# Performance work log

Measured on AMD Instinct MI355X. Metric: run time of the kernel, lower is better.

The kernel has to match this reference:

```python
import jax, jax.numpy as jnp
import numpy as np

EPS = 1e-12          # sinkhorn_knopp epsilon
LOW, HIGH = 0.02, 0.98  # SquashedSigmoid bounds
N_ITERS = 10         # num_iterations
BATCH = 2097152


def setup_inputs() -> dict:
    key = jax.random.key(0)
    ks = jax.random.split(key, 9)
    dims = [6, 64, 32, 16, 9]
    inp = {"margins": jax.random.uniform(ks[0], (BATCH, 6), jnp.float32, 0.05, 1.0)}
    for i in range(4):
        fi, fo = dims[i], dims[i + 1]
        inp[f"W{i+1}"] = jax.random.normal(ks[1 + 2 * i], (fi, fo), jnp.float32) / np.float32(np.sqrt(fi))
        inp[f"b{i+1}"] = jnp.zeros((fo,), jnp.float32)
    return inp


def _mlp(x, W1, b1, W2, b2, W3, b3, W4, b4):
    h = jax.nn.relu(x @ W1 + b1)
    h = jax.nn.relu(h @ W2 + b2)
    h = jax.nn.relu(h @ W3 + b3)
    return h @ W4 + b4  # [B, 9]


def _tau(p4):
    # user-supplied tau: 4 positive params -> 3x3 matrix; 2x2 block padded with ones
    B = p4.shape[0]
    A = jnp.ones((B, 3, 3), p4.dtype)
    return A.at[:, :2, :2].set(p4.reshape(B, 2, 2))


def _sinkhorn_knopp(A, r, c):
    # batched row/col balancing; per-sample A is 3x3, r/c are length-3 margins
    for _ in range(N_ITERS):
        A = A * (r[:, :, None] / (A.sum(axis=2, keepdims=True) + EPS))
        A = A * (c[:, None, :] / (A.sum(axis=1, keepdims=True) + EPS))
    return A


def reference(margins, W1, b1, W2, b2, W3, b3, W4, b4):
    B = margins.shape[0]
    M, F = margins[:, 0:3], margins[:, 3:6]
    pars = _mlp(margins, W1, b1, W2, b2, W3, b3, W4, b4)
    muc = _tau(jnp.exp(pars[:, 0:4]))                     # [B,3,3]
    sqs = lambda x: LOW + (HIGH - LOW) * jax.nn.sigmoid(x)
    shm, shf = sqs(pars[:, 4:6]), sqs(pars[:, 6:8])
    V = jnp.exp(pars[:, -1])                              # [B]
    ones = jnp.ones((B, 1), margins.dtype)
    shm0 = jnp.concatenate([shm, ones], axis=1)           # [B,3]
    shf0 = jnp.concatenate([shf, ones], axis=1)
    mucm0, muc0f = M * shm0, F * shf0                     # row / col margins
    mum0, mu0f = M * (1 - shm0), F * (1 - shf0)
    muc = _sinkhorn_knopp(muc, mucm0, muc0f)              # [B,3,3]
    top = jnp.concatenate([muc, mum0[:, :, None]], axis=2)                    # [B,3,4]
    bot = jnp.concatenate([mu0f[:, None, :], jnp.zeros((B, 1, 1), margins.dtype)], axis=2)  # [B,1,4]
    mus = jnp.concatenate([top, bot], axis=1)             # [B,4,4]
    return (mus, V)
```

## Files before the change

kernel.cpp:

```cpp
#include <hip/hip_runtime.h>

typedef _Float16 f16x8 __attribute__((ext_vector_type(8)));
typedef _Float16 f16x4 __attribute__((ext_vector_type(4)));
typedef float    f32x4 __attribute__((ext_vector_type(4)));

static constexpr float kLOW  = 0.02f;
static constexpr float kHIGH = 0.98f;

__device__ __forceinline__ float fast_rcp(float v) {
    return __builtin_amdgcn_rcpf(v);
}
__device__ __forceinline__ float fast_sigmoid(float v) {
    return fast_rcp(1.0f + __expf(-v));
}

enum : int {
    WS_A1 = 0,
    WS_A2 = 4096,
    WS_A3 = 8192,
    WS_A4 = 9216,
    WS_B1 = 10240,
    WS_B2 = 14336,
    WS_B3 = 16384,
    WS_B4 = 17408,
    WS_TOTAL = 18432
};

__global__ __launch_bounds__(256) void prep_frags(
    const float* __restrict__ W1, const float* __restrict__ b1,
    const float* __restrict__ W2, const float* __restrict__ b2,
    const float* __restrict__ W3, const float* __restrict__ b3,
    const float* __restrict__ W4, const float* __restrict__ b4,
    char* __restrict__ ws)
{
    const int lane = threadIdx.x & 63;
    const int wid  = threadIdx.x >> 6;
    const int n16  = lane & 15;
    const int q    = lane >> 4;

    if (wid == 0) {
#pragma unroll
        for (int mt = 0; mt < 4; ++mt) {
            f16x8 a;
#pragma unroll
            for (int j = 0; j < 8; ++j) a[j] = (_Float16)0.0f;
            if (q == 0) {
#pragma unroll
                for (int j = 0; j < 6; ++j)
                    a[j] = (_Float16)W1[j * 64 + mt * 16 + n16];
            }
            ((f16x8*)(ws + WS_A1))[mt * 64 + lane] = a;
        }
#pragma unroll
        for (int mt = 0; mt < 4; ++mt)
            ((f32x4*)(ws + WS_B1))[mt * 64 + lane] = *(const f32x4*)(b1 + mt * 16 + q * 4);
    } else if (wid == 1) {
#pragma unroll
        for (int mt = 0; mt < 2; ++mt)
#pragma unroll
            for (int kt = 0; kt < 2; ++kt) {
                f16x8 a;
#pragma unroll
                for (int j = 0; j < 8; ++j)
                    a[j] = (_Float16)W2[(kt * 32 + q * 8 + j) * 32 + mt * 16 + n16];
                ((f16x8*)(ws + WS_A2))[(mt * 2 + kt) * 64 + lane] = a;
            }
    } else if (wid == 2) {
        f16x8 a3;
#pragma unroll
        for (int j = 0; j < 8; ++j)
            a3[j] = (_Float16)W3[(q * 8 + j) * 16 + n16];
        ((f16x8*)(ws + WS_A3))[lane] = a3;
        f16x8 a4;
#pragma unroll
        for (int j = 0; j < 8; ++j) {
            const int k = q * 8 + j;
            a4[j] = (k < 16 && n16 < 9) ? (_Float16)W4[k * 9 + n16] : (_Float16)0.0f;
        }
        ((f16x8*)(ws + WS_A4))[lane] = a4;
    } else {
#pragma unroll
        for (int mt = 0; mt < 2; ++mt)
            ((f32x4*)(ws + WS_B2))[mt * 64 + lane] = *(const f32x4*)(b2 + mt * 16 + q * 4);
        ((f32x4*)(ws + WS_B3))[lane] = *(const f32x4*)(b3 + q * 4);
        f32x4 bb;
#pragma unroll
        for (int r = 0; r < 4; ++r) {
            const int m = q * 4 + r;
            bb[r] = (m < 9) ? b4[m] : 0.0f;
        }
        ((f32x4*)(ws + WS_B4))[lane] = bb;
    }
}

__global__ __launch_bounds__(256, 4) void sinkhorn_mlp_mfma(
    const float* __restrict__ margins, const char* __restrict__ ws,
    float* __restrict__ out_mus, float* __restrict__ out_V, int B)
{
    __shared__ __align__(16) char smem_all[4 * 9216];
    const int lane = threadIdx.x & 63;
    const int wid  = threadIdx.x >> 6;
    char* smem = smem_all + wid * 9216;

    const int n16 = lane & 15;
    const int q   = lane >> 4;

    const int row  = blockIdx.x * 256 + wid * 64 + lane;
    const int rowC = row < B ? row : (B - 1);

    float x[6];
    {
        const float2* mp = (const float2*)(margins + (size_t)rowC * 6);
        const float2 a = mp[0], b = mp[1], c = mp[2];
        x[0] = a.x; x[1] = a.y; x[2] = b.x; x[3] = b.y; x[4] = c.x; x[5] = c.y;
    }

    {
        f16x8 xr;
#pragma unroll
        for (int j = 0; j < 8; ++j) xr[j] = (_Float16)0.0f;
#pragma unroll
        for (int i = 0; i < 6; ++i) xr[i] = (_Float16)x[i];
        *(f16x8*)(smem + 8176 + lane * 16) = xr;
        if (lane == 0) {
            f16x8 z;
#pragma unroll
            for (int j = 0; j < 8; ++j) z[j] = (_Float16)0.0f;
            *(f16x8*)(smem + 9200) = z;
        }
    }

    f16x8 A1[4], A2w[2][2], A3w, A4w;
#pragma unroll
    for (int mt = 0; mt < 4; ++mt) A1[mt] = ((const f16x8*)(ws + WS_A1))[mt * 64 + lane];
#pragma unroll
    for (int mt = 0; mt < 2; ++mt)
#pragma unroll
        for (int kt = 0; kt < 2; ++kt)
            A2w[mt][kt] = ((const f16x8*)(ws + WS_A2))[(mt * 2 + kt) * 64 + lane];
    A3w = ((const f16x8*)(ws + WS_A3))[lane];
    A4w = ((const f16x8*)(ws + WS_A4))[lane];

    f32x4 b1v[4], b2v[2], b3v, b4v;
#pragma unroll
    for (int mt = 0; mt < 4; ++mt) b1v[mt] = ((const f32x4*)(ws + WS_B1))[mt * 64 + lane];
#pragma unroll
    for (int mt = 0; mt < 2; ++mt) b2v[mt] = ((const f32x4*)(ws + WS_B2))[mt * 64 + lane];
    b3v = ((const f32x4*)(ws + WS_B3))[lane];
    b4v = ((const f32x4*)(ws + WS_B4))[lane];

    f16x8 BX[4];
    {
        const int xo   = (q == 0) ? (8176 + n16 * 16) : 9200;
        const int step = (q == 0) ? 256 : 0;
#pragma unroll
        for (int nt = 0; nt < 4; ++nt)
            BX[nt] = *(const f16x8*)(smem + xo + nt * step);
    }
#pragma unroll
    for (int mt = 0; mt < 4; ++mt) {
#pragma unroll
        for (int nt = 0; nt < 4; ++nt) {
            f32x4 C = b1v[mt];
            C = __builtin_amdgcn_mfma_f32_16x16x32_f16(A1[mt], BX[nt], C, 0, 0, 0);
            f16x4 hv;
#pragma unroll
            for (int r = 0; r < 4; ++r) hv[r] = (_Float16)fmaxf(C[r], 0.0f);
            *(f16x4*)(smem + (nt*16 + n16) * 144 + mt*32 + q*8) = hv;
        }
    }

    f16x8 H1f[4][2];
#pragma unroll
    for (int nt = 0; nt < 4; ++nt)
#pragma unroll
        for (int kt = 0; kt < 2; ++kt)
            H1f[nt][kt] = *(const f16x8*)(smem + (nt*16 + n16) * 144 + kt*64 + q*16);
#pragma unroll
    for (int mt = 0; mt < 2; ++mt) {
#pragma unroll
        for (int nt = 0; nt < 4; ++nt) {
            f32x4 C = b2v[mt];
            C = __builtin_amdgcn_mfma_f32_16x16x32_f16(A2w[mt][0], H1f[nt][0], C, 0, 0, 0);
            C = __builtin_amdgcn_mfma_f32_16x16x32_f16(A2w[mt][1], H1f[nt][1], C, 0, 0, 0);
            f16x4 hv;
#pragma unroll
            for (int r = 0; r < 4; ++r) hv[r] = (_Float16)fmaxf(C[r], 0.0f);
            *(f16x4*)(smem + (nt*16 + n16) * 80 + mt*32 + q*8) = hv;
        }
    }

    f16x8 H2f[4];
#pragma unroll
    for (int nt = 0; nt < 4; ++nt)
        H2f[nt] = *(const f16x8*)(smem + (nt*16 + n16) * 80 + q*16);
#pragma unroll
    for (int nt = 0; nt < 4; ++nt) {
        f32x4 C = b3v;
        C = __builtin_amdgcn_mfma_f32_16x16x32_f16(A3w, H2f[nt], C, 0, 0, 0);
        f16x4 hv;
#pragma unroll
        for (int r = 0; r < 4; ++r) hv[r] = (_Float16)fmaxf(C[r], 0.0f);
        *(f16x4*)(smem + (nt*16 + n16) * 32 + q*8) = hv;
    }

    f16x8 B4[4];
#pragma unroll
    for (int nt = 0; nt < 4; ++nt) {
        const int off = (q < 2) ? ((nt*16 + n16) * 32 + q * 16) : 9200;
        B4[nt] = *(const f16x8*)(smem + off);
    }
#pragma unroll
    for (int nt = 0; nt < 4; ++nt) {
        f32x4 C = b4v;
        C = __builtin_amdgcn_mfma_f32_16x16x32_f16(A4w, B4[nt], C, 0, 0, 0);
        *(f32x4*)(smem + 2560 + (nt*16 + n16) * 80 + q * 16) = C;
    }

    float p[9];
    {
        const char* pr = smem + 2560 + lane * 80;
        *(f32x4*)&p[0] = *(const f32x4*)(pr);
        *(f32x4*)&p[4] = *(const f32x4*)(pr + 16);
        p[8] = *(const float*)(pr + 32);
    }

    const float K00 = __expf(p[0]), K01 = __expf(p[1]);
    const float K10 = __expf(p[2]), K11 = __expf(p[3]);

    const float sh_m0 = kLOW + (kHIGH - kLOW) * fast_sigmoid(p[4]);
    const float sh_m1 = kLOW + (kHIGH - kLOW) * fast_sigmoid(p[5]);
    const float sh_f0 = kLOW + (kHIGH - kLOW) * fast_sigmoid(p[6]);
    const float sh_f1 = kLOW + (kHIGH - kLOW) * fast_sigmoid(p[7]);
    const float V = __expf(p[8]);

    const float M0 = x[0], M1 = x[1], M2 = x[2];
    const float F0 = x[3], F1 = x[4], F2 = x[5];

    const float r0 = M0 * sh_m0, r1 = M1 * sh_m1, r2 = M2;
    const float c0 = F0 * sh_f0, c1 = F1 * sh_f1, c2 = F2;
    const float mum0_0 = M0 * (1.0f - sh_m0), mum0_1 = M1 * (1.0f - sh_m1);
    const float mu0f_0 = F0 * (1.0f - sh_f0), mu0f_1 = F1 * (1.0f - sh_f1);

    const float rc2 = fast_rcp(c2);
    const float g0 = c0 * rc2, g1 = c1 * rc2;
    float v0 = 1.0f, v1 = 1.0f;
    float u0, u1, u2;
#pragma unroll
    for (int it = 0; it < 9; ++it) {
        const float s0 = fmaf(K00, v0, fmaf(K01, v1, 1.0f));
        const float s1 = fmaf(K10, v0, fmaf(K11, v1, 1.0f));
        const float s2 = v0 + v1 + 1.0f;
        u0 = r0 * fast_rcp(s0);
        u1 = r1 * fast_rcp(s1);
        u2 = r2 * fast_rcp(s2);
        const float t0 = fmaf(K00, u0, fmaf(K10, u1, u2));
        const float t1 = fmaf(K01, u0, fmaf(K11, u1, u2));
        const float t2 = u0 + u1 + u2;
        v0 = g0 * (t2 * fast_rcp(t0));
        v1 = g1 * (t2 * fast_rcp(t1));
    }
    float vf0, vf1, vf2;
    {
        const float s0 = fmaf(K00, v0, fmaf(K01, v1, 1.0f));
        const float s1 = fmaf(K10, v0, fmaf(K11, v1, 1.0f));
        const float s2 = v0 + v1 + 1.0f;
        u0 = r0 * fast_rcp(s0);
        u1 = r1 * fast_rcp(s1);
        u2 = r2 * fast_rcp(s2);
        const float t0 = fmaf(K00, u0, fmaf(K10, u1, u2));
        const float t1 = fmaf(K01, u0, fmaf(K11, u1, u2));
        const float t2 = u0 + u1 + u2;
        vf0 = c0 * fast_rcp(t0);
        vf1 = c1 * fast_rcp(t1);
        vf2 = c2 * fast_rcp(t2);
    }
    const float A00 = u0 * K00 * vf0, A01 = u0 * K01 * vf1, A02 = u0 * vf2;
    const float A10 = u1 * K10 * vf0, A11 = u1 * K11 * vf1, A12 = u1 * vf2;
    const float A20 = u2 * vf0,       A21 = u2 * vf1,       A22 = u2 * vf2;

    if (row < B) {
        float4* o = (float4*)(out_mus + (size_t)row * 16);
        o[0] = make_float4(A00, A01, A02, mum0_0);
        o[1] = make_float4(A10, A11, A12, mum0_1);
        o[2] = make_float4(A20, A21, A22, 0.0f);
        o[3] = make_float4(mu0f_0, mu0f_1, 0.0f, 0.0f);
        out_V[row] = V;
    }
}

extern "C" void kernel_launch(void* const* d_in, const int* in_sizes, int n_in,
                              void* d_out, int out_size, void* d_ws, size_t ws_size,
                              hipStream_t stream) {
    const float* margins = (const float*)d_in[0];
    const float* W1 = (const float*)d_in[1];
    const float* b1 = (const float*)d_in[2];
    const float* W2 = (const float*)d_in[3];
    const float* b2 = (const float*)d_in[4];
    const float* W3 = (const float*)d_in[5];
    const float* b3 = (const float*)d_in[6];
    const float* W4 = (const float*)d_in[7];
    const float* b4 = (const float*)d_in[8];

    const int B = in_sizes[0] / 6;
    float* out_mus = (float*)d_out;
    float* out_V   = out_mus + (size_t)B * 16;
    char*  ws      = (char*)d_ws;

    hipLaunchKernelGGL(prep_frags, dim3(1), dim3(256), 0, stream,
                       W1, b1, W2, b2, W3, b3, W4, b4, ws);

    dim3 block(256);
    dim3 grid((B + 255) / 256);
    hipLaunchKernelGGL(sinkhorn_mlp_mfma, grid, block, 0, stream,
                       margins, ws, out_mus, out_V, B);
}
```

Before: 224.5 us.

## Shrink per-wave LDS with XOR swizzle, packed ReLU converts, higher occupancy

After: 270.8 us. 20.6% more time.

```diff
diff --git a/kernel.cpp b/kernel.cpp
--- a/kernel.cpp
+++ b/kernel.cpp
@@ -2,6 +2,7 @@
 
 typedef _Float16 f16x8 __attribute__((ext_vector_type(8)));
 typedef _Float16 f16x4 __attribute__((ext_vector_type(4)));
+typedef __fp16   fp16x2 __attribute__((ext_vector_type(2)));
 typedef float    f32x4 __attribute__((ext_vector_type(4)));
 
 static constexpr float kLOW  = 0.02f;
@@ -12,6 +13,10 @@
 }
 __device__ __forceinline__ float fast_sigmoid(float v) {
     return fast_rcp(1.0f + __expf(-v));
+}
+__device__ __forceinline__ unsigned int relu_pk(float a, float b) {
+    fp16x2 r = __builtin_amdgcn_cvt_pkrtz(fmaxf(a, 0.0f), fmaxf(b, 0.0f));
+    return __builtin_bit_cast(unsigned int, r);
 }
 
 enum : int {
@@ -93,14 +98,14 @@
     }
 }
 
-__global__ __launch_bounds__(256, 4) void sinkhorn_mlp_mfma(
+__global__ __launch_bounds__(256, 5) void sinkhorn_mlp_mfma(
     const float* __restrict__ margins, const char* __restrict__ ws,
     float* __restrict__ out_mus, float* __restrict__ out_V, int B)
 {
-    __shared__ __align__(16) char smem_all[4 * 9216];
+    __shared__ __align__(16) char smem_all[4 * 8192];
     const int lane = threadIdx.x & 63;
     const int wid  = threadIdx.x >> 6;
-    char* smem = smem_all + wid * 9216;
+    char* smem = smem_all + wid * 8192;
 
     const int n16 = lane & 15;
     const int q   = lane >> 4;
@@ -121,13 +126,7 @@
         for (int j = 0; j < 8; ++j) xr[j] = (_Float16)0.0f;
 #pragma unroll
         for (int i = 0; i < 6; ++i) xr[i] = (_Float16)x[i];
-        *(f16x8*)(smem + 8176 + lane * 16) = xr;
-        if (lane == 0) {
-            f16x8 z;
-#pragma unroll
-            for (int j = 0; j < 8; ++j) z[j] = (_Float16)0.0f;
-            *(f16x8*)(smem + 9200) = z;
-        }
+        *(f16x8*)(smem + 7168 + lane * 16) = xr;
     }
 
     f16x8 A1[4], A2w[2][2], A3w, A4w;
@@ -150,12 +149,15 @@
     b4v = ((const f32x4*)(ws + WS_B4))[lane];
 
     f16x8 BX[4];
-    {
-        const int xo   = (q == 0) ? (8176 + n16 * 16) : 9200;
-        const int step = (q == 0) ? 256 : 0;
+    if (q == 0) {
 #pragma unroll
         for (int nt = 0; nt < 4; ++nt)
-            BX[nt] = *(const f16x8*)(smem + xo + nt * step);
+            BX[nt] = *(const f16x8*)(smem + 7168 + (nt * 16 + n16) * 16);
+    } else {
+#pragma unroll
+        for (int nt = 0; nt < 4; ++nt)
+#pragma unroll
+            for (int j = 0; j < 8; ++j) BX[nt][j] = (_Float16)0.0f;
     }
 #pragma unroll
     for (int mt = 0; mt < 4; ++mt) {
@@ -163,19 +165,25 @@
         for (int nt = 0; nt < 4; ++nt) {
             f32x4 C = b1v[mt];
             C = __builtin_amdgcn_mfma_f32_16x16x32_f16(A1[mt], BX[nt], C, 0, 0, 0);
-            f16x4 hv;
-#pragma unroll
-            for (int r = 0; r < 4; ++r) hv[r] = (_Float16)fmaxf(C[r], 0.0f);
-            *(f16x4*)(smem + (nt*16 + n16) * 144 + mt*32 + q*8) = hv;
+            uint2 hv;
+            hv.x = relu_pk(C[0], C[1]);
+            hv.y = relu_pk(C[2], C[3]);
+            const int r = nt * 16 + n16;
+            const int col = (mt * 32 + q * 8) ^ ((r & 7) << 4);
+            *(uint2*)(smem + r * 128 + col) = hv;
         }
     }
 
     f16x8 H1f[4][2];
 #pragma unroll
-    for (int nt = 0; nt < 4; ++nt)
-#pragma unroll
-        for (int kt = 0; kt < 2; ++kt)
-            H1f[nt][kt] = *(const f16x8*)(smem + (nt*16 + n16) * 144 + kt*64 + q*16);
+    for (int nt = 0; nt < 4; ++nt) {
+        const int r = nt * 16 + n16;
+#pragma unroll
+        for (int kt = 0; kt < 2; ++kt) {
+            const int col = (kt * 64 + q * 16) ^ ((r & 7) << 4);
+            H1f[nt][kt] = *(const f16x8*)(smem + r * 128 + col);
+        }
+    }
 #pragma unroll
     for (int mt = 0; mt < 2; ++mt) {
 #pragma unroll
@@ -183,10 +191,10 @@
             f32x4 C = b2v[mt];
             C = __builtin_amdgcn_mfma_f32_16x16x32_f16(A2w[mt][0], H1f[nt][0], C, 0, 0, 0);
             C = __builtin_amdgcn_mfma_f32_16x16x32_f16(A2w[mt][1], H1f[nt][1], C, 0, 0, 0);
-            f16x4 hv;
-#pragma unroll
-            for (int r = 0; r < 4; ++r) hv[r] = (_Float16)fmaxf(C[r], 0.0f);
-            *(f16x4*)(smem + (nt*16 + n16) * 80 + mt*32 + q*8) = hv;
+            uint2 hv;
+            hv.x = relu_pk(C[0], C[1]);
+            hv.y = relu_pk(C[2], C[3]);
+            *(uint2*)(smem + (nt*16 + n16) * 80 + mt*32 + q*8) = hv;
         }
     }
 
@@ -205,10 +213,15 @@
     }
 
     f16x8 B4[4];
-#pragma unroll
-    for (int nt = 0; nt < 4; ++nt) {
-        const int off = (q < 2) ? ((nt*16 + n16) * 32 + q * 16) : 9200;
-        B4[nt] = *(const f16x8*)(smem + off);
+    if (q < 2) {
+#pragma unroll
+        for (int nt = 0; nt < 4; ++nt)
+            B4[nt] = *(const f16x8*)(smem + (nt*16 + n16) * 32 + q * 16);
+    } else {
+#pragma unroll
+        for (int nt = 0; nt < 4; ++nt)
+#pragma unroll
+            for (int j = 0; j < 8; ++j) B4[nt][j] = (_Float16)0.0f;
     }
 #pragma unroll
     for (int nt = 0; nt < 4; ++nt) {
```
